# Optimization experiments

Measured on AMD Instinct MI355X. Metric: run time of the kernel, lower is better.

The kernel has to match this reference:

```python
import jax, jax.numpy as jnp
import numpy as np

N, D, Q, C_IN, C = 8192, 32, 4096, 128, 256
EPS = 1e-5

def _bn(h, g, b):
    # training-mode BatchNorm1d (biased variance, as torch uses for normalization)
    mu = h.mean(0)
    var = ((h - mu) ** 2).mean(0)
    return (h - mu) * jax.lax.rsqrt(var + EPS) * g + b

def setup_inputs():
    key = jax.random.key(0)
    cnt = iter(range(1000))
    def w(shape, s=0.05):
        return jax.random.normal(jax.random.fold_in(key, next(cnt)), shape, jnp.float32) * s
    ones = lambda n: jnp.ones((n,), jnp.float32)
    zeros = lambda n: jnp.zeros((n,), jnp.float32)
    rng = np.random.default_rng(0)
    block = N // D
    # padded neighbor table: rows sorted & duplicate-free (one neighbor per id-block)
    nbr_np = (np.arange(D)[None, :] * block + rng.integers(0, block, size=(N, D))).astype(np.int64)
    src = np.repeat(np.arange(N, dtype=np.int64), D)
    edge_index = jnp.asarray(np.stack([src, nbr_np.reshape(-1)]))
    E = edge_index.shape[1]
    C2 = 2 * C
    return {
        'x': w((N, C_IN), 1.0),
        'edge_index': edge_index,
        'edge_weight': jax.random.uniform(jax.random.fold_in(key, 999), (E,), jnp.float32, 0.5, 1.5),
        'edge_label_index': jnp.asarray(rng.integers(0, N, size=(2, Q)).astype(np.int64)),
        'nbr': jnp.asarray(nbr_np),
        'pe_gamma': ones(C_IN), 'pe_beta': zeros(C_IN),
        'W_pe': w((C_IN, C)), 'b_pe': zeros(C),
        'W_gcn': w((C, C)), 'b_gcn': zeros(C), 'bn1_g': ones(C), 'bn1_b': zeros(C),
        'Wq': w((C, C)), 'bq': zeros(C), 'Wk': w((C, C)), 'bk': zeros(C),
        'Wv': w((C, C)), 'bv': zeros(C), 'Wo': w((C, C)), 'bo': zeros(C),
        'bn2_g': ones(C), 'bn2_b': zeros(C),
        'W_m1': w((C, C2)), 'b_m1': zeros(C2), 'W_m2': w((C2, C)), 'b_m2': zeros(C),
        'bn3_g': ones(C), 'bn3_b': zeros(C),
        'W_cm': w((C, C)), 'b_cm': zeros(C), 'W_sm': w((C, C)), 'b_sm': zeros(C),
        'W_o1': w((C2, C)), 'b_o1': zeros(C), 'bno_g': ones(C), 'bno_b': zeros(C),
        'W_o2': w((C, 1)), 'b_o2': zeros(1),
        't': jnp.ones((), jnp.float32),
    }

def reference(x, edge_index, edge_weight, edge_label_index, nbr,
              pe_gamma, pe_beta, W_pe, b_pe,
              W_gcn, b_gcn, bn1_g, bn1_b,
              Wq, bq, Wk, bk, Wv, bv, Wo, bo, bn2_g, bn2_b,
              W_m1, b_m1, W_m2, b_m2, bn3_g, bn3_b,
              W_cm, b_cm, W_sm, b_sm,
              W_o1, b_o1, bno_g, bno_b, W_o2, b_o2, t):
    src, dst = edge_index[0], edge_index[1]
    h = _bn(x, pe_gamma, pe_beta) @ W_pe + b_pe                       # [N, C]
    # --- GPSConv layer: local GCN (self-loops) + global attention + MLP ---
    deg = jnp.zeros((N,), h.dtype).at[dst].add(edge_weight) + 1.0     # self-loop weight 1
    dinv = jax.lax.rsqrt(deg)
    hw = h @ W_gcn
    coef = dinv[src] * edge_weight * dinv[dst]
    agg = jnp.zeros_like(hw).at[dst].add(hw[src] * coef[:, None])
    local = agg + hw * (dinv * dinv)[:, None] + b_gcn
    h1 = _bn(local + h, bn1_g, bn1_b)
    q = h @ Wq + bq; k = h @ Wk + bk; v = h @ Wv + bv
    attn = jax.nn.softmax((q @ k.T) / jnp.sqrt(jnp.float32(C)), axis=-1)  # [N, N]
    h2 = _bn((attn @ v) @ Wo + bo + h, bn2_g, bn2_b)
    z = h1 + h2
    z = _bn(z + jax.nn.relu(z @ W_m1 + b_m1) @ W_m2 + b_m2, bn3_g, bn3_b)  # content features
    # --- structure: common-neighbor intersection + per-channel softmax aggregation ---
    s_nbr = nbr[edge_label_index[1]]        # [Q, D] sorted neighbors of source
    t_nbr = nbr[edge_label_index[0]]        # [Q, D] sorted neighbors of target
    pos = jnp.minimum(jax.vmap(jnp.searchsorted)(s_nbr, t_nbr), D - 1)
    mask = jnp.take_along_axis(s_nbr, pos, axis=1) == t_nbr           # common-neighbor mask
    zg = z[t_nbr]                           # [Q, D, C]
    m3 = mask[:, :, None]
    scores = jnp.where(m3, t * zg, -1e30)
    e = jnp.where(m3, jnp.exp(scores - jnp.max(scores, axis=1, keepdims=True)), 0.0)
    alpha = e / jnp.maximum(e.sum(axis=1, keepdims=True), 1e-12)
    structure = (alpha * zg).sum(axis=1)    # [Q, C]; zero rows when no common nbrs
    # --- predictor ---
    content = z[edge_label_index[0]] * z[edge_label_index[1]]
    hcat = jnp.concatenate([content @ W_cm + b_cm, structure @ W_sm + b_sm], axis=-1)
    hmid = jax.nn.relu(_bn(hcat @ W_o1 + b_o1, bno_g, bno_b))
    return hmid @ W_o2 + b_o2               # [Q, 1]
```

## Files before the change

kernel.cpp:

```cpp
#include <hip/hip_runtime.h>
#include <hip/hip_bf16.h>

using bf16 = __hip_bfloat16;
typedef __attribute__((ext_vector_type(8))) short short8;
typedef __attribute__((ext_vector_type(4))) float f32x4;
typedef __attribute__((ext_vector_type(4))) unsigned short us4;

#define NN 8192
#define DD 32
#define QQ 4096
#define CINN 128
#define CH 256
#define EE (NN*DD)
#define MBYTE ((size_t)1024*1024)
#define KB ((size_t)1024)

__device__ __forceinline__ short f2bf(float f){
  bf16 h = __float2bfloat16(f);
  return *reinterpret_cast<short*>(&h);
}
__device__ __forceinline__ float bf2f(unsigned short s){
  unsigned int u = ((unsigned int)s) << 16;
  return __uint_as_float(u);
}
__device__ __forceinline__ void gl_lds16(const void* g, void* l){
  __builtin_amdgcn_global_load_lds(
      (const __attribute__((address_space(1))) void*)g,
      (__attribute__((address_space(3))) void*)l, 16, 0, 0);
}

__global__ void k_prep(float* stats, int nstats, int* cnt,
                       const float* __restrict__ bq, const float* __restrict__ bk,
                       const float* __restrict__ bv, float* __restrict__ bcat){
  int i = blockIdx.x*256 + threadIdx.x;
  if (i < 1024){
    float v = 0.f;
    if (i >= 768)      v = bv[i-768];
    else if (i >= 512) v = bk[i-512];
    else if (i >= 256) v = bq[i-256]*0.0625f;
    bcat[i] = v;
  }
  int j = i - 1024;
  if (j >= 0 && j < nstats) stats[j] = 0.f;
  int k2 = j - nstats;
  if (k2 >= 0 && k2 < NN) cnt[k2] = 0;
}

struct WPack {
  const float* src[11];
  bf16* dst[11];
  int K[11];
  int N[11];
  float sc[11];
  int cum[12];
};
__global__ void k_wconv_all(WPack p){
  int idx = blockIdx.x*256 + threadIdx.x;
  if (idx >= p.cum[11]) return;
  int w = 0;
#pragma unroll
  for (int i = 1; i < 11; i++) w += (idx >= p.cum[i]) ? 1 : 0;
  int loc = idx - p.cum[w];
  int K = p.K[w], N = p.N[w];
  int n = loc / K, k = loc - n*K;
  p.dst[w][loc] = __float2bfloat16(p.src[w][(size_t)k*N + n] * p.sc[w]);
}

__global__ void k_bnstats(const float* __restrict__ X, float* __restrict__ sums, int M, int C){
  int c = threadIdx.x;
  float s = 0.f, s2 = 0.f;
  for (int r = blockIdx.x; r < M; r += gridDim.x){
    float v = X[(size_t)r*C + c];
    s += v; s2 += v*v;
  }
  atomicAdd(&sums[c], s);
  atomicAdd(&sums[C+c], s2);
}

__global__ void k_bnapply(const float* __restrict__ X, const float* __restrict__ sums,
                          const float* __restrict__ g, const float* __restrict__ b,
                          const float* __restrict__ addin, const bf16* __restrict__ addinb,
                          float* __restrict__ outf, bf16* __restrict__ outb,
                          int M, int Cm1, int relu){
  int idx = blockIdx.x*256 + threadIdx.x;
  int c = idx & Cm1;
  int C = Cm1 + 1;
  float mu = sums[c] / (float)M;
  float var = sums[C+c] / (float)M - mu*mu;
  float rs = rsqrtf(var + 1e-5f);
  float v = (X[idx] - mu)*rs*g[c] + b[c];
  if (addin) v += addin[idx];
  if (addinb) v += __bfloat162float(addinb[idx]);
  if (relu) v = fmaxf(v, 0.f);
  if (outf) outf[idx] = v;
  if (outb) outb[idx] = __float2bfloat16(v);
}

template<int KCH>
__global__ __launch_bounds__(256)
void k_gemm(const bf16* __restrict__ A, const bf16* __restrict__ BT,
            const float* __restrict__ bias,
            const float* __restrict__ resid, const bf16* __restrict__ residb,
            float* __restrict__ Cf, bf16* __restrict__ Cb,
            int Ncols, int ldc, int relu,
            const bf16* __restrict__ A2, const bf16* __restrict__ BT2,
            const float* __restrict__ bias2, int half, int colbase2,
            float* __restrict__ stats)
{
  constexpr int K = KCH*32;
  int bid = blockIdx.x;
  const bf16* Ause = A;
  const bf16* BTu = BT;
  const float* bi = bias;
  int colbase = 0;
  if (A2 && bid >= half){ Ause = A2; BTu = BT2; bi = bias2; bid -= half; colbase = colbase2; }
  const int row0 = bid*16;
  const int wid = threadIdx.x >> 6;
  const int lane = threadIdx.x & 63;
  const int lr = lane & 15, lg = lane >> 4;
  short8 af[KCH];
  const short* Arow = (const short*)Ause + (size_t)(row0+lr)*K + lg*8;
#pragma unroll
  for (int c2 = 0; c2 < KCH; c2++) af[c2] = *(const short8*)(Arow + c2*32);
  const int ntiles = Ncols >> 4;
  for (int ct = wid; ct < ntiles; ct += 4){
    f32x4 acc = {0.f,0.f,0.f,0.f};
    const short* Brow = (const short*)BTu + (size_t)(ct*16+lr)*K + lg*8;
#pragma unroll
    for (int c2 = 0; c2 < KCH; c2++){
      short8 bfr = *(const short8*)(Brow + c2*32);
      acc = __builtin_amdgcn_mfma_f32_16x16x32_bf16(af[c2], bfr, acc, 0, 0, 0);
    }
    int col = colbase + ct*16 + lr;
    float bvv = bi ? bi[ct*16+lr] : 0.f;
    float vv[4];
#pragma unroll
    for (int r = 0; r < 4; r++){
      int row = row0 + lg*4 + r;
      size_t o = (size_t)row*ldc + col;
      float v = acc[r] + bvv;
      if (resid) v += resid[o];
      if (residb) v += __bfloat162float(residb[o]);
      if (relu) v = fmaxf(v, 0.f);
      if (Cf) Cf[o] = v;
      if (Cb) Cb[o] = __float2bfloat16(v);
      vv[r] = v;
    }
    if (stats){
      float s  = vv[0]+vv[1]+vv[2]+vv[3];
      float s2 = vv[0]*vv[0]+vv[1]*vv[1]+vv[2]*vv[2]+vv[3]*vv[3];
      s  += __shfl_xor(s, 16, 64);  s  += __shfl_xor(s, 32, 64);
      s2 += __shfl_xor(s2, 16, 64); s2 += __shfl_xor(s2, 32, 64);
      if (lg == 0){
        atomicAdd(&stats[col], s);
        atomicAdd(&stats[CH + col], s2);
      }
    }
  }
}

template<int KCH>
__global__ __launch_bounds__(256)
void k_gemm2(const bf16* __restrict__ A, const bf16* __restrict__ BT,
             const float* __restrict__ bias,
             const float* __restrict__ resid, const bf16* __restrict__ residb,
             float* __restrict__ Cf, bf16* __restrict__ Cb,
             int ncolsh, int ldc, int relu,
             int halfblocks, int colshift,
             float* __restrict__ stats)
{
  constexpr int K = KCH*32;
  int bid = blockIdx.x;
  int colbase = 0;
  if (bid >= halfblocks){ bid -= halfblocks; colbase = colshift; }
  const int row0 = bid*32;
  const int wid = threadIdx.x >> 6;
  const int lane = threadIdx.x & 63;
  const int lr = lane & 15, lg = lane >> 4;
  short8 af0[KCH], af1[KCH];
  const short* Arow0 = (const short*)A + (size_t)(row0+lr)*K + lg*8;
  const short* Arow1 = Arow0 + 16*K;
#pragma unroll
  for (int c2 = 0; c2 < KCH; c2++){
    af0[c2] = *(const short8*)(Arow0 + c2*32);
    af1[c2] = *(const short8*)(Arow1 + c2*32);
  }
  const int ntiles = ncolsh >> 4;
  for (int ct = wid; ct < ntiles; ct += 4){
    f32x4 a0 = {0.f,0.f,0.f,0.f}, a1 = {0.f,0.f,0.f,0.f};
    const short* Brow = (const short*)BT + (size_t)(colbase + ct*16 + lr)*K + lg*8;
#pragma unroll
    for (int c2 = 0; c2 < KCH; c2++){
      short8 bfr = *(const short8*)(Brow + c2*32);
      a0 = __builtin_amdgcn_mfma_f32_16x16x32_bf16(af0[c2], bfr, a0, 0, 0, 0);
      a1 = __builtin_amdgcn_mfma_f32_16x16x32_bf16(af1[c2], bfr, a1, 0, 0, 0);
    }
    int col = colbase + ct*16 + lr;
    float bvv = bias ? bias[col] : 0.f;
    float vv0[4], vv1[4];
#pragma unroll
    for (int r = 0; r < 4; r++){
      int row = row0 + lg*4 + r;
      size_t o0 = (size_t)row*ldc + col;
      size_t o1 = (size_t)(row+16)*ldc + col;
      float v0 = a0[r] + bvv;
      float v1 = a1[r] + bvv;
      if (resid){ v0 += resid[o0]; v1 += resid[o1]; }
      if (residb){ v0 += __bfloat162float(residb[o0]); v1 += __bfloat162float(residb[o1]); }
      if (relu){ v0 = fmaxf(v0, 0.f); v1 = fmaxf(v1, 0.f); }
      if (Cf){ Cf[o0] = v0; Cf[o1] = v1; }
      if (Cb){ Cb[o0] = __float2bfloat16(v0); Cb[o1] = __float2bfloat16(v1); }
      vv0[r] = v0; vv1[r] = v1;
    }
    if (stats){
      float s  = vv0[0]+vv0[1]+vv0[2]+vv0[3] + vv1[0]+vv1[1]+vv1[2]+vv1[3];
      float s2 = vv0[0]*vv0[0]+vv0[1]*vv0[1]+vv0[2]*vv0[2]+vv0[3]*vv0[3]
               + vv1[0]*vv1[0]+vv1[1]*vv1[1]+vv1[2]*vv1[2]+vv1[3]*vv1[3];
      s  += __shfl_xor(s, 16, 64);  s  += __shfl_xor(s, 32, 64);
      s2 += __shfl_xor(s2, 16, 64); s2 += __shfl_xor(s2, 32, 64);
      if (lg == 0){
        atomicAdd(&stats[col], s);
        atomicAdd(&stats[CH + col], s2);
      }
    }
  }
}

__global__ void k_hist(const int* __restrict__ dst, int* __restrict__ cnt){
  int e = blockIdx.x*256 + threadIdx.x;
  if (e < EE) atomicAdd(&cnt[dst[e]], 1);
}

__global__ void k_scan(const int* __restrict__ cnt, int* __restrict__ off, int* __restrict__ woff){
  __shared__ int s[256];
  int t = threadIdx.x;
  int base = t*32;
  int local[32];
  int sum = 0;
#pragma unroll
  for (int i = 0; i < 32; i++){ local[i] = sum; sum += cnt[base+i]; }
  s[t] = sum;
  __syncthreads();
  if (t == 0){
    int run = 0;
    for (int i = 0; i < 256; i++){ int v = s[i]; s[i] = run; run += v; }
  }
  __syncthreads();
  int b = s[t];
#pragma unroll
  for (int i = 0; i < 32; i++){ off[base+i] = b + local[i]; woff[base+i] = b + local[i]; }
  if (t == 255) off[8192] = EE;
}

__global__ void k_fill(const int* __restrict__ dst, int* __restrict__ woff, int* __restrict__ elist){
  int e = blockIdx.x*256 + threadIdx.x;
  if (e < EE){
    int p = atomicAdd(&woff[dst[e]], 1);
    elist[p] = e;
  }
}

__global__ __launch_bounds__(256)
void k_degcsr(const int* __restrict__ off, const int* __restrict__ elist,
              const float* __restrict__ ew, float* __restrict__ dinv){
  int n = blockIdx.x*4 + (threadIdx.x >> 6);
  int lane = threadIdx.x & 63;
  int o0 = off[n], o1 = off[n+1];
  float s = 0.f;
  for (int j = o0 + lane; j < o1; j += 64) s += ew[elist[j]];
#pragma unroll
  for (int o = 32; o; o >>= 1) s += __shfl_xor(s, o, 64);
  if (lane == 0) dinv[n] = rsqrtf(s + 1.0f);
}

__global__ __launch_bounds__(256)
void k_gather(const int* __restrict__ off, const int* __restrict__ elist,
              const float* __restrict__ ew, const float* __restrict__ dinv,
              const unsigned short* __restrict__ hwq, const unsigned short* __restrict__ hb16,
              const float* __restrict__ bgcn, float* __restrict__ y1){
  int n = blockIdx.x*4 + (threadIdx.x >> 6);
  int lane = threadIdx.x & 63;
  int o0 = off[n], o1 = off[n+1];
  float dn = dinv[n];
  f32x4 acc = {0.f,0.f,0.f,0.f};
  for (int j = o0; j < o1; j++){
    int e = elist[j];
    int s = e >> 5;
    float coef = dinv[s]*ew[e]*dn;
    us4 v = *(const us4*)(hwq + (size_t)s*1024 + lane*4);
    acc[0] += bf2f(v[0])*coef; acc[1] += bf2f(v[1])*coef;
    acc[2] += bf2f(v[2])*coef; acc[3] += bf2f(v[3])*coef;
  }
  us4 hv = *(const us4*)(hwq + (size_t)n*1024 + lane*4);
  us4 hn = *(const us4*)(hb16 + (size_t)n*CH + lane*4);
  f32x4 bg  = ((const f32x4*)bgcn)[lane];
  float dd = dn*dn;
  f32x4 o;
  o[0] = acc[0] + bf2f(hv[0])*dd + bg[0] + bf2f(hn[0]);
  o[1] = acc[1] + bf2f(hv[1])*dd + bg[1] + bf2f(hn[1]);
  o[2] = acc[2] + bf2f(hv[2])*dd + bg[2] + bf2f(hn[2]);
  o[3] = acc[3] + bf2f(hv[3])*dd + bg[3] + bf2f(hn[3]);
  ((f32x4*)(y1 + (size_t)n*CH))[lane] = o;
}

__global__ __launch_bounds__(256)
void k_transpose(const bf16* __restrict__ in, bf16* __restrict__ out, int istride){
  __shared__ short tile[32][33];
  int bx = blockIdx.x & 7;
  int by = blockIdx.x >> 3;
  int tx = threadIdx.x & 31, ty = threadIdx.x >> 5;
  const short* inp = (const short*)in;
  short* outp = (short*)out;
#pragma unroll
  for (int i = 0; i < 4; i++)
    tile[ty + i*8][tx] = inp[(size_t)(by*32 + ty + i*8)*istride + bx*32 + tx];
  __syncthreads();
#pragma unroll
  for (int i = 0; i < 4; i++)
    outp[(size_t)(bx*32 + ty + i*8)*8192 + by*32 + tx] = tile[tx][ty + i*8];
}

__global__ __launch_bounds__(256, 2)
void k_attn9(const bf16* __restrict__ QKV, const bf16* __restrict__ VT,
             bf16* __restrict__ Opart, float* __restrict__ Lpart)
{
  __shared__ char lds[75776];
  const int wid = threadIdx.x >> 6, lane = threadIdx.x & 63;
  const int lr = lane & 15, lg = lane >> 4;
  const int qt = blockIdx.x >> 3, sp = blockIdx.x & 7;
  const int q0 = qt*128 + wid*32;
  const int kbase = sp*1024;
  const float M0 = 8.f;

  short8 qf[2][8];
#pragma unroll
  for (int qs = 0; qs < 2; qs++){
    const short* Qrow = (const short*)QKV + 256 + (size_t)(q0 + qs*16 + lr)*1024 + lg*8;
#pragma unroll
    for (int c = 0; c < 8; c++) qf[qs][c] = *(const short8*)(Qrow + c*32);
  }

  const char* kS[4];
  const char* vS[4];
  int ldst[4];
#pragma unroll
  for (int i = 0; i < 4; i++){
    int L = wid*1024 + i*4096 + lane*16;
    int r = L >> 9, b = L & 511;
    kS[i] = (const char*)QKV + (size_t)(kbase + r)*2048 + 1024 + (b ^ ((r&7)<<4));
    int j = L >> 7, b2 = L & 127;
    int bp2 = b2 ^ ((j&7)<<4);
    int dim = 2*j + (bp2 >= 64 ? 1 : 0);
    vS[i] = (const char*)VT + ((size_t)dim*8192 + kbase)*2 + (bp2 & 63);
    ldst[i] = wid*1024 + i*4096;
  }

  f32x4 acc[2][16];
#pragma unroll
  for (int qs = 0; qs < 2; qs++)
#pragma unroll
    for (int dt = 0; dt < 16; dt++) acc[qs][dt] = {0.f,0.f,0.f,0.f};
  float ls[2][4];
#pragma unroll
  for (int qs = 0; qs < 2; qs++)
#pragma unroll
    for (int r = 0; r < 4; r++) ls[qs][r] = 0.f;

  char* sPw = lds + 65536 + wid*2560;

#pragma unroll
  for (int i = 0; i < 4; i++){
    gl_lds16(kS[i], lds + ldst[i]);           kS[i] += 65536;
    gl_lds16(vS[i], lds + 16384 + ldst[i]);   vS[i] += 64;
  }
  __syncthreads();

  for (int t = 0; t < 32; t++){
    const int buf = t & 1;
    if (t < 31){
      char* nb = lds + (buf^1)*32768;
#pragma unroll
      for (int i = 0; i < 4; i++){
        gl_lds16(kS[i], nb + ldst[i]);           kS[i] += 65536;
        gl_lds16(vS[i], nb + 16384 + ldst[i]);   vS[i] += 64;
      }
    }
    const char* bK = lds + buf*32768;
    const char* bV = bK + 16384;

    {
      f32x4 s0 = {0.f,0.f,0.f,0.f}, s1 = {0.f,0.f,0.f,0.f};
      __builtin_amdgcn_s_setprio(1);
#pragma unroll
      for (int c = 0; c < 8; c++){
        int g = c*64 + lg*16;
        short8 kf0 = *(const short8*)(bK + lr*512 + (g ^ ((lr&7)<<4)));
        s0 = __builtin_amdgcn_mfma_f32_16x16x32_bf16(qf[0][c], kf0, s0, 0, 0, 0);
        short8 kf1 = *(const short8*)(bK + (16+lr)*512 + (g ^ ((lr&7)<<4)));
        s1 = __builtin_amdgcn_mfma_f32_16x16x32_bf16(qf[0][c], kf1, s1, 0, 0, 0);
      }
      __builtin_amdgcn_s_setprio(0);
#pragma unroll
      for (int r = 0; r < 4; r++){
        float p0 = __expf(s0[r] - M0);
        float p1 = __expf(s1[r] - M0);
        ls[0][r] += p0 + p1;
        int prow = lg*4 + r;
        *(short*)(sPw + prow*80 + lr*2)      = f2bf(p0);
        *(short*)(sPw + prow*80 + 32 + lr*2) = f2bf(p1);
      }
    }
    {
      f32x4 s0 = {0.f,0.f,0.f,0.f}, s1 = {0.f,0.f,0.f,0.f};
      __builtin_amdgcn_s_setprio(1);
#pragma unroll
      for (int c = 0; c < 8; c++){
        int g = c*64 + lg*16;
        short8 kf0 = *(const short8*)(bK + lr*512 + (g ^ ((lr&7)<<4)));
        s0 = __builtin_amdgcn_mfma_f32_16x16x32_bf16(qf[1][c], kf0, s0, 0, 0, 0);
        short8 kf1 = *(const short8*)(bK + (16+lr)*512 + (g ^ ((lr&7)<<4)));
        s1 = __builtin_amdgcn_mfma_f32_16x16x32_bf16(qf[1][c], kf1, s1, 0, 0, 0);
      }
      __builtin_amdgcn_s_setprio(0);
#pragma unroll
      for (int r = 0; r < 4; r++){
        float p0 = __expf(s0[r] - M0);
        float p1 = __expf(s1[r] - M0);
        ls[1][r] += p0 + p1;
        int prow = lg*4 + r;
        *(short*)(sPw + 1280 + prow*80 + lr*2)      = f2bf(p0);
        *(short*)(sPw + 1280 + prow*80 + 32 + lr*2) = f2bf(p1);
      }
    }
    __builtin_amdgcn_sched_barrier(0);
    short8 pf0 = *(const short8*)(sPw + lr*80 + lg*16);
    short8 pf1 = *(const short8*)(sPw + 1280 + lr*80 + lg*16);
    __builtin_amdgcn_s_setprio(1);
#pragma unroll
    for (int dt = 0; dt < 16; dt++){
      int d = dt*16 + lr;
      int j = d >> 1;
      int gp = (d&1)*64 + lg*16;
      short8 vf = *(const short8*)(bV + j*128 + (gp ^ ((j&7)<<4)));
      acc[0][dt] = __builtin_amdgcn_mfma_f32_16x16x32_bf16(pf0, vf, acc[0][dt], 0, 0, 0);
      acc[1][dt] = __builtin_amdgcn_mfma_f32_16x16x32_bf16(pf1, vf, acc[1][dt], 0, 0, 0);
    }
    __builtin_amdgcn_s_setprio(0);
    __syncthreads();
  }

#pragma unroll
  for (int qs = 0; qs < 2; qs++){
#pragma unroll
    for (int r = 0; r < 4; r++){
#pragma unroll
      for (int off = 1; off < 16; off <<= 1) ls[qs][r] += __shfl_xor(ls[qs][r], off, 64);
    }
  }
  if (lr == 0){
#pragma unroll
    for (int qs = 0; qs < 2; qs++){
#pragma unroll
      for (int r = 0; r < 4; r++){
        int row = q0 + qs*16 + lg*4 + r;
        Lpart[sp*NN + row] = ls[qs][r];
      }
    }
  }
  char* reg = lds + wid*8192;
  size_t ob = (size_t)sp*NN*CH;
#pragma unroll
  for (int qs = 0; qs < 2; qs++){
#pragma unroll
    for (int dt = 0; dt < 16; dt++){
#pragma unroll
      for (int r = 0; r < 4; r++){
        int qr = lg*4 + r;
        *(short*)(reg + qr*512 + ((dt*32 + lr*2) ^ ((qr&7)<<4))) = f2bf(acc[qs][dt][r]);
      }
    }
    __syncthreads();
#pragma unroll
    for (int rnd = 0; rnd < 8; rnd++){
      int qr = rnd*2 + (lane >> 5);
      int colb = (lane & 31)*16;
      short8 v = *(const short8*)(reg + qr*512 + (colb ^ ((qr&7)<<4)));
      *(short8*)((short*)Opart + ob + (size_t)(q0 + qs*16 + qr)*CH + colb/2) = v;
    }
    __syncthreads();
  }
}

__global__ __launch_bounds__(256)
void k_merge8(const bf16* __restrict__ Opart, const float* __restrict__ Lp,
              bf16* __restrict__ out){
  int tid = blockIdx.x*256 + threadIdx.x;
  int q = tid >> 5;
  int cb = (tid & 31) * 8;
  float den = 0.f;
#pragma unroll
  for (int s = 0; s < 8; s++) den += Lp[s*NN + q];
  float inv = 1.f / den;
  float o[8];
#pragma unroll
  for (int j = 0; j < 8; j++) o[j] = 0.f;
#pragma unroll
  for (int s = 0; s < 8; s++){
    short8 v = *(const short8*)((const short*)Opart + (size_t)s*NN*CH + (size_t)q*CH + cb);
#pragma unroll
    for (int j = 0; j < 8; j++) o[j] += bf2f((unsigned short)v[j]);
  }
  short8 res;
#pragma unroll
  for (int j = 0; j < 8; j++) res[j] = f2bf(o[j]*inv);
  *(short8*)((short*)out + (size_t)q*CH + cb) = res;
}

__global__ __launch_bounds__(256)
void k_head(const int* __restrict__ eli, const int* __restrict__ nbr,
            const float* __restrict__ y3, const float* __restrict__ stat3,
            const float* __restrict__ g3, const float* __restrict__ b3,
            const float* __restrict__ tptr,
            bf16* __restrict__ outc, bf16* __restrict__ outs){
  __shared__ int tn[32];
  __shared__ int msk[32];
  int q = blockIdx.x;
  int a0 = eli[q], b0 = eli[QQ + q];
  if (threadIdx.x < 32){
    int d = threadIdx.x;
    int a = nbr[(size_t)a0*DD + d];
    int s = nbr[(size_t)b0*DD + d];
    tn[d] = a;
    msk[d] = (a == s);
  }
  __syncthreads();
  int c = threadIdx.x;
  float mu = stat3[c] / (float)NN;
  float var = stat3[CH + c] / (float)NN - mu*mu;
  float rs = rsqrtf(var + 1e-5f);
  float sc = rs*g3[c];
  float sh = b3[c] - mu*sc;
  float za = y3[(size_t)a0*CH + c]*sc + sh;
  float zb = y3[(size_t)b0*CH + c]*sc + sh;
  outc[(size_t)q*CH + c] = __float2bfloat16(za*zb);
  float tval = tptr[0];
  float vmax = -1e30f;
  float zg[32];
#pragma unroll
  for (int d = 0; d < 32; d++){
    float v = msk[d] ? (y3[(size_t)tn[d]*CH + c]*sc + sh) : 0.f;
    zg[d] = v;
    float scv = msk[d] ? tval*v : -1e30f;
    vmax = fmaxf(vmax, scv);
  }
  float esum = 0.f, wsum = 0.f;
#pragma unroll
  for (int d = 0; d < 32; d++){
    float e = msk[d] ? __expf(tval*zg[d] - vmax) : 0.f;
    esum += e;
    wsum += e*zg[d];
  }
  outs[(size_t)q*CH + c] = __float2bfloat16(wsum / fmaxf(esum, 1e-12f));
}

__global__ __launch_bounds__(256)
void k_final(const bf16* __restrict__ hmid, const float* __restrict__ w,
             const float* __restrict__ b, float* __restrict__ out){
  int r = blockIdx.x*4 + (threadIdx.x >> 6);
  int lane = threadIdx.x & 63;
  float s = 0.f;
#pragma unroll
  for (int i = 0; i < 4; i++){
    int c = lane + 64*i;
    s += __bfloat162float(hmid[(size_t)r*CH + c]) * w[c];
  }
#pragma unroll
  for (int off = 32; off; off >>= 1) s += __shfl_xor(s, off, 64);
  if (lane == 0) out[r] = s + b[0];
}

extern "C" void kernel_launch(void* const* d_in, const int* in_sizes, int n_in,
                              void* d_out, int out_size, void* d_ws, size_t ws_size,
                              hipStream_t stream)
{
  const float* x      = (const float*)d_in[0];
  const int*   eidx   = (const int*)d_in[1];
  const float* ew     = (const float*)d_in[2];
  const int*   eli    = (const int*)d_in[3];
  const int*   nbr    = (const int*)d_in[4];
  const float* pe_g   = (const float*)d_in[5];
  const float* pe_b   = (const float*)d_in[6];
  const float* W_pe   = (const float*)d_in[7];
  const float* b_pe   = (const float*)d_in[8];
  const float* W_gcn  = (const float*)d_in[9];
  const float* b_gcn  = (const float*)d_in[10];
  const float* bn1_g  = (const float*)d_in[11];
  const float* bn1_b  = (const float*)d_in[12];
  const float* Wq     = (const float*)d_in[13];
  const float* bq     = (const float*)d_in[14];
  const float* Wk     = (const float*)d_in[15];
  const float* bk     = (const float*)d_in[16];
  const float* Wv     = (const float*)d_in[17];
  const float* bvv    = (const float*)d_in[18];
  const float* Wo     = (const float*)d_in[19];
  const float* bo     = (const float*)d_in[20];
  const float* bn2_g  = (const float*)d_in[21];
  const float* bn2_b  = (const float*)d_in[22];
  const float* W_m1   = (const float*)d_in[23];
  const float* b_m1   = (const float*)d_in[24];
  const float* W_m2   = (const float*)d_in[25];
  const float* b_m2   = (const float*)d_in[26];
  const float* bn3_g  = (const float*)d_in[27];
  const float* bn3_b  = (const float*)d_in[28];
  const float* W_cm   = (const float*)d_in[29];
  const float* b_cm   = (const float*)d_in[30];
  const float* W_sm   = (const float*)d_in[31];
  const float* b_sm   = (const float*)d_in[32];
  const float* W_o1   = (const float*)d_in[33];
  const float* b_o1   = (const float*)d_in[34];
  const float* bno_g  = (const float*)d_in[35];
  const float* bno_b  = (const float*)d_in[36];
  const float* W_o2   = (const float*)d_in[37];
  const float* b_o2   = (const float*)d_in[38];
  const float* tptr   = (const float*)d_in[39];

  if (ws_size < 64*MBYTE) return;
  char* ws = (char*)d_ws;

  bf16* WgcnT = (bf16*)(ws + 0);
  bf16* WqT   = (bf16*)(ws + 128*KB);
  bf16* WkT   = (bf16*)(ws + 256*KB);
  bf16* WvT   = (bf16*)(ws + 384*KB);
  bf16* WpeT  = (bf16*)(ws + 512*KB);
  bf16* Wm1T  = (bf16*)(ws + 576*KB);
  bf16* Wm2T  = (bf16*)(ws + 832*KB);
  bf16* WcmT  = (bf16*)(ws + 1088*KB);
  bf16* WsmT  = (bf16*)(ws + 1216*KB);
  bf16* Wo1T  = (bf16*)(ws + 1344*KB);
  bf16* WoT   = (bf16*)(ws + 1600*KB);

  float* stat_x = (float*)(ws + 2*MBYTE);
  float* stat1  = (float*)(ws + 2*MBYTE + 1*KB);
  float* stat2  = (float*)(ws + 2*MBYTE + 3*KB);
  float* stat3  = (float*)(ws + 2*MBYTE + 5*KB);
  float* stato  = (float*)(ws + 2*MBYTE + 7*KB);
  float* deg    = (float*)(ws + 2*MBYTE + 16*KB);
  float* bcat   = (float*)(ws + 2*MBYTE + 64*KB);
  int*   cnt    = (int*)(ws + 2*MBYTE + 128*KB);
  int*   off    = (int*)(ws + 2*MBYTE + 160*KB);
  int*   woff   = (int*)(ws + 2*MBYTE + 224*KB);
  int*   elist  = (int*)(ws + 2*MBYTE + 288*KB);
  float* Lpart  = (float*)(ws + 2*MBYTE + 1664*KB);

  bf16*  hb    = (bf16*)(ws + 4*MBYTE);
  bf16*  xn    = (bf16*)(ws + 8*MBYTE);
  float* aggb  = (float*)(ws + 10*MBYTE);
  bf16*  OpartB= (bf16*)(ws + 8*MBYTE);
  bf16*  vT    = (bf16*)(ws + 40*MBYTE);
  bf16*  qkvg  = (bf16*)(ws + 44*MBYTE);
  bf16*  h1b   = (bf16*)(ws + 60*MBYTE);
  bf16*  attnb = (bf16*)(ws + 40*MBYTE);
  float* y2    = (float*)(ws + 8*MBYTE);
  float* zf    = (float*)(ws + 16*MBYTE);
  bf16*  zb    = (bf16*)(ws + 24*MBYTE);
  bf16*  midb  = (bf16*)(ws + 28*MBYTE);
  float* y3    = (float*)(ws + 44*MBYTE);
  bf16*  contb = (bf16*)(ws + 8*MBYTE);
  bf16*  strub = (bf16*)(ws + 10*MBYTE);
  bf16*  hcat  = (bf16*)(ws + 12*MBYTE);
  float* y4    = (float*)(ws + 16*MBYTE);
  bf16*  hmid  = (bf16*)(ws + 20*MBYTE);

  const int* dstp = eidx + EE;

  k_prep<<<(1024 + 12288 + NN + 255)/256, 256, 0, stream>>>((float*)(ws + 2*MBYTE), 12288, cnt, bq, bk, bvv, bcat);

  {
    WPack p;
    const float* s[11] = {W_gcn, Wq, Wk, Wv, W_pe, W_m1, W_m2, W_cm, W_sm, W_o1, Wo};
    bf16* dsts[11] = {WgcnT, WqT, WkT, WvT, WpeT, Wm1T, Wm2T, WcmT, WsmT, Wo1T, WoT};
    int Ks[11] = {256,256,256,256,128,256,512,256,256,512,256};
    int Ns[11] = {256,256,256,256,256,512,256,256,256,256,256};
    float scs[11] = {1.f,0.0625f,1.f,1.f,1.f,1.f,1.f,1.f,1.f,1.f,1.f};
    int c = 0;
    for (int i = 0; i < 11; i++){
      p.src[i]=s[i]; p.dst[i]=dsts[i]; p.K[i]=Ks[i]; p.N[i]=Ns[i]; p.sc[i]=scs[i];
      p.cum[i]=c; c += Ks[i]*Ns[i];
    }
    p.cum[11]=c;
    k_wconv_all<<<(c+255)/256, 256, 0, stream>>>(p);
  }

  k_hist<<<EE/256, 256, 0, stream>>>(dstp, cnt);
  k_scan<<<1, 256, 0, stream>>>(cnt, off, woff);
  k_fill<<<EE/256, 256, 0, stream>>>(dstp, woff, elist);
  k_degcsr<<<NN/4, 256, 0, stream>>>(off, elist, ew, deg);

  k_bnstats<<<256, 128, 0, stream>>>(x, stat_x, NN, CINN);
  k_bnapply<<<NN*CINN/256, 256, 0, stream>>>(x, stat_x, pe_g, pe_b, nullptr, nullptr, nullptr, xn, NN, CINN-1, 0);

  k_gemm2<4><<<512, 256, 0, stream>>>(xn, WpeT, b_pe, nullptr, nullptr, nullptr, hb, 128, 256, 0,
                                       256, 128, nullptr);

  k_gemm2<8><<<512, 256, 0, stream>>>(hb, WgcnT, bcat, nullptr, nullptr, nullptr, qkvg, 512, 1024, 0,
                                       256, 512, nullptr);

  k_gather<<<NN/4, 256, 0, stream>>>(off, elist, ew, deg,
                                      (const unsigned short*)qkvg, (const unsigned short*)hb, b_gcn, aggb);

  k_bnstats<<<256, 256, 0, stream>>>(aggb, stat1, NN, CH);
  k_bnapply<<<NN*CH/256, 256, 0, stream>>>(aggb, stat1, bn1_g, bn1_b, nullptr, nullptr, nullptr, h1b, NN, CH-1, 0);

  k_transpose<<<2048, 256, 0, stream>>>(qkvg + 768, vT, 1024);

  k_attn9<<<512, 256, 0, stream>>>(qkvg, vT, OpartB, Lpart);
  k_merge8<<<NN*32/256, 256, 0, stream>>>(OpartB, Lpart, attnb);

  k_gemm2<8><<<512, 256, 0, stream>>>(attnb, WoT, bo, nullptr, hb, y2, nullptr, 128, 256, 0,
                                       256, 128, stat2);

  k_bnapply<<<NN*CH/256, 256, 0, stream>>>(y2, stat2, bn2_g, bn2_b, nullptr, h1b, zf, zb, NN, CH-1, 0);

  k_gemm2<8><<<512, 256, 0, stream>>>(zb, Wm1T, b_m1, nullptr, nullptr, nullptr, midb, 256, 512, 1,
                                       256, 256, nullptr);
  k_gemm2<16><<<512, 256, 0, stream>>>(midb, Wm2T, b_m2, zf, nullptr, y3, nullptr, 128, 256, 0,
                                        256, 128, stat3);

  k_head<<<QQ, 256, 0, stream>>>(eli, nbr, y3, stat3, bn3_g, bn3_b, tptr, contb, strub);

  k_gemm<8><<<2*(QQ/16), 256, 0, stream>>>(contb, WcmT, b_cm, nullptr, nullptr, nullptr, hcat, 256, 512, 0,
                                            strub, WsmT, b_sm, QQ/16, 256, nullptr);

  k_gemm2<16><<<256, 256, 0, stream>>>(hcat, Wo1T, b_o1, nullptr, nullptr, y4, nullptr, 128, 256, 0,
                                        128, 128, stato);
  k_bnapply<<<QQ*CH/256, 256, 0, stream>>>(y4, stato, bno_g, bno_b, nullptr, nullptr, nullptr, hmid, QQ, CH-1, 1);

  k_final<<<QQ/4, 256, 0, stream>>>(hmid, W_o2, b_o2, (float*)d_out);
}
```

Measured before the change: 376.2 us.

## Fuse prep kernels, defer BN1 into z kernel, fold final BN into head

Merges the prep and weight-conversion launches into one kernel. The GCN gather now writes bf16 instead of fp32, and its BN stats are read from bf16. BN1 is no longer applied in its own pass: it is applied together with BN2 and the residual inside a new k_bnz kernel. The last BN+ReLU is folded into k_final, and the MLP residual now reads bf16 z instead of fp32 z. This removes several launches and full-tensor round trips, at the cost of extra bf16 rounding on the aggregated features and the residual.

```diff
diff --git a/kernel.cpp b/kernel.cpp
--- a/kernel.cpp
+++ b/kernel.cpp
@@ -29,23 +29,6 @@
       (__attribute__((address_space(3))) void*)l, 16, 0, 0);
 }
 
-__global__ void k_prep(float* stats, int nstats, int* cnt,
-                       const float* __restrict__ bq, const float* __restrict__ bk,
-                       const float* __restrict__ bv, float* __restrict__ bcat){
-  int i = blockIdx.x*256 + threadIdx.x;
-  if (i < 1024){
-    float v = 0.f;
-    if (i >= 768)      v = bv[i-768];
-    else if (i >= 512) v = bk[i-512];
-    else if (i >= 256) v = bq[i-256]*0.0625f;
-    bcat[i] = v;
-  }
-  int j = i - 1024;
-  if (j >= 0 && j < nstats) stats[j] = 0.f;
-  int k2 = j - nstats;
-  if (k2 >= 0 && k2 < NN) cnt[k2] = 0;
-}
-
 struct WPack {
   const float* src[11];
   bf16* dst[11];
@@ -54,12 +37,27 @@
   float sc[11];
   int cum[12];
 };
-__global__ void k_wconv_all(WPack p){
-  int idx = blockIdx.x*256 + threadIdx.x;
+__global__ void k_prepw(WPack p, float* stats, int nstats, int* cnt,
+                        const float* __restrict__ bq, const float* __restrict__ bk,
+                        const float* __restrict__ bv, float* __restrict__ bcat){
+  int i = blockIdx.x*256 + threadIdx.x;
+  if (i < 1024){
+    float v = 0.f;
+    if (i >= 768)      v = bv[i-768];
+    else if (i >= 512) v = bk[i-512];
+    else if (i >= 256) v = bq[i-256]*0.0625f;
+    bcat[i] = v;
+    return;
+  }
+  int j = i - 1024;
+  if (j < nstats){ stats[j] = 0.f; return; }
+  int k2 = j - nstats;
+  if (k2 < NN){ cnt[k2] = 0; return; }
+  int idx = k2 - NN;
   if (idx >= p.cum[11]) return;
   int w = 0;
 #pragma unroll
-  for (int i = 1; i < 11; i++) w += (idx >= p.cum[i]) ? 1 : 0;
+  for (int t = 1; t < 11; t++) w += (idx >= p.cum[t]) ? 1 : 0;
   int loc = idx - p.cum[w];
   int K = p.K[w], N = p.N[w];
   int n = loc / K, k = loc - n*K;
@@ -77,11 +75,20 @@
   atomicAdd(&sums[C+c], s2);
 }
 
+__global__ void k_bnstats_b(const bf16* __restrict__ X, float* __restrict__ sums, int M, int C){
+  int c = threadIdx.x;
+  float s = 0.f, s2 = 0.f;
+  for (int r = blockIdx.x; r < M; r += gridDim.x){
+    float v = __bfloat162float(X[(size_t)r*C + c]);
+    s += v; s2 += v*v;
+  }
+  atomicAdd(&sums[c], s);
+  atomicAdd(&sums[C+c], s2);
+}
+
 __global__ void k_bnapply(const float* __restrict__ X, const float* __restrict__ sums,
                           const float* __restrict__ g, const float* __restrict__ b,
-                          const float* __restrict__ addin, const bf16* __restrict__ addinb,
-                          float* __restrict__ outf, bf16* __restrict__ outb,
-                          int M, int Cm1, int relu){
+                          bf16* __restrict__ outb, int M, int Cm1){
   int idx = blockIdx.x*256 + threadIdx.x;
   int c = idx & Cm1;
   int C = Cm1 + 1;
@@ -89,23 +96,34 @@
   float var = sums[C+c] / (float)M - mu*mu;
   float rs = rsqrtf(var + 1e-5f);
   float v = (X[idx] - mu)*rs*g[c] + b[c];
-  if (addin) v += addin[idx];
-  if (addinb) v += __bfloat162float(addinb[idx]);
-  if (relu) v = fmaxf(v, 0.f);
-  if (outf) outf[idx] = v;
-  if (outb) outb[idx] = __float2bfloat16(v);
+  outb[idx] = __float2bfloat16(v);
+}
+
+__global__ void k_bnz(const float* __restrict__ y2, const float* __restrict__ stat2,
+                      const float* __restrict__ g2, const float* __restrict__ b2,
+                      const bf16* __restrict__ y1b, const float* __restrict__ stat1,
+                      const float* __restrict__ g1, const float* __restrict__ b1,
+                      bf16* __restrict__ zb){
+  int idx = blockIdx.x*256 + threadIdx.x;
+  int c = idx & 255;
+  float mu2 = stat2[c] / (float)NN;
+  float var2 = stat2[CH+c] / (float)NN - mu2*mu2;
+  float rs2 = rsqrtf(var2 + 1e-5f);
+  float v2 = (y2[idx] - mu2)*rs2*g2[c] + b2[c];
+  float mu1 = stat1[c] / (float)NN;
+  float var1 = stat1[CH+c] / (float)NN - mu1*mu1;
+  float rs1 = rsqrtf(var1 + 1e-5f);
+  float v1 = (__bfloat162float(y1b[idx]) - mu1)*rs1*g1[c] + b1[c];
+  zb[idx] = __float2bfloat16(v1 + v2);
 }
 
 template<int KCH>
 __global__ __launch_bounds__(256)
 void k_gemm(const bf16* __restrict__ A, const bf16* __restrict__ BT,
             const float* __restrict__ bias,
-            const float* __restrict__ resid, const bf16* __restrict__ residb,
-            float* __restrict__ Cf, bf16* __restrict__ Cb,
-            int Ncols, int ldc, int relu,
+            bf16* __restrict__ Cb, int ldc,
             const bf16* __restrict__ A2, const bf16* __restrict__ BT2,
-            const float* __restrict__ bias2, int half, int colbase2,
-            float* __restrict__ stats)
+            const float* __restrict__ bias2, int half, int colbase2)
 {
   constexpr int K = KCH*32;
   int bid = blockIdx.x;
@@ -122,7 +140,7 @@
   const short* Arow = (const short*)Ause + (size_t)(row0+lr)*K + lg*8;
 #pragma unroll
   for (int c2 = 0; c2 < KCH; c2++) af[c2] = *(const short8*)(Arow + c2*32);
-  const int ntiles = Ncols >> 4;
+  const int ntiles = 256 >> 4;
   for (int ct = wid; ct < ntiles; ct += 4){
     f32x4 acc = {0.f,0.f,0.f,0.f};
     const short* Brow = (const short*)BTu + (size_t)(ct*16+lr)*K + lg*8;
@@ -133,28 +151,12 @@
     }
     int col = colbase + ct*16 + lr;
     float bvv = bi ? bi[ct*16+lr] : 0.f;
-    float vv[4];
 #pragma unroll
     for (int r = 0; r < 4; r++){
       int row = row0 + lg*4 + r;
       size_t o = (size_t)row*ldc + col;
       float v = acc[r] + bvv;
-      if (resid) v += resid[o];
-      if (residb) v += __bfloat162float(residb[o]);
-      if (relu) v = fmaxf(v, 0.f);
-      if (Cf) Cf[o] = v;
-      if (Cb) Cb[o] = __float2bfloat16(v);
-      vv[r] = v;
-    }
-    if (stats){
-      float s  = vv[0]+vv[1]+vv[2]+vv[3];
-      float s2 = vv[0]*vv[0]+vv[1]*vv[1]+vv[2]*vv[2]+vv[3]*vv[3];
-      s  += __shfl_xor(s, 16, 64);  s  += __shfl_xor(s, 32, 64);
-      s2 += __shfl_xor(s2, 16, 64); s2 += __shfl_xor(s2, 32, 64);
-      if (lg == 0){
-        atomicAdd(&stats[col], s);
-        atomicAdd(&stats[CH + col], s2);
-      }
+      Cb[o] = __float2bfloat16(v);
     }
   }
 }
@@ -277,7 +279,7 @@
 void k_gather(const int* __restrict__ off, const int* __restrict__ elist,
               const float* __restrict__ ew, const float* __restrict__ dinv,
               const unsigned short* __restrict__ hwq, const unsigned short* __restrict__ hb16,
-              const float* __restrict__ bgcn, float* __restrict__ y1){
+              const float* __restrict__ bgcn, bf16* __restrict__ y1b){
   int n = blockIdx.x*4 + (threadIdx.x >> 6);
   int lane = threadIdx.x & 63;
   int o0 = off[n], o1 = off[n+1];
@@ -295,12 +297,12 @@
   us4 hn = *(const us4*)(hb16 + (size_t)n*CH + lane*4);
   f32x4 bg  = ((const f32x4*)bgcn)[lane];
   float dd = dn*dn;
-  f32x4 o;
-  o[0] = acc[0] + bf2f(hv[0])*dd + bg[0] + bf2f(hn[0]);
-  o[1] = acc[1] + bf2f(hv[1])*dd + bg[1] + bf2f(hn[1]);
-  o[2] = acc[2] + bf2f(hv[2])*dd + bg[2] + bf2f(hn[2]);
-  o[3] = acc[3] + bf2f(hv[3])*dd + bg[3] + bf2f(hn[3]);
-  ((f32x4*)(y1 + (size_t)n*CH))[lane] = o;
+  us4 o;
+  o[0] = (unsigned short)f2bf(acc[0] + bf2f(hv[0])*dd + bg[0] + bf2f(hn[0]));
+  o[1] = (unsigned short)f2bf(acc[1] + bf2f(hv[1])*dd + bg[1] + bf2f(hn[1]));
+  o[2] = (unsigned short)f2bf(acc[2] + bf2f(hv[2])*dd + bg[2] + bf2f(hn[2]));
+  o[3] = (unsigned short)f2bf(acc[3] + bf2f(hv[3])*dd + bg[3] + bf2f(hn[3]));
+  *(us4*)((unsigned short*)y1b + (size_t)n*CH + lane*4) = o;
 }
 
 __global__ __launch_bounds__(256)
@@ -564,19 +566,26 @@
 }
 
 __global__ __launch_bounds__(256)
-void k_final(const bf16* __restrict__ hmid, const float* __restrict__ w,
-             const float* __restrict__ b, float* __restrict__ out){
+void k_final(const float* __restrict__ y4, const float* __restrict__ stato,
+             const float* __restrict__ g, const float* __restrict__ b,
+             const float* __restrict__ w, const float* __restrict__ bo2,
+             float* __restrict__ out){
   int r = blockIdx.x*4 + (threadIdx.x >> 6);
   int lane = threadIdx.x & 63;
   float s = 0.f;
 #pragma unroll
   for (int i = 0; i < 4; i++){
     int c = lane + 64*i;
-    s += __bfloat162float(hmid[(size_t)r*CH + c]) * w[c];
+    float mu = stato[c] / (float)QQ;
+    float var = stato[CH+c] / (float)QQ - mu*mu;
+    float rs = rsqrtf(var + 1e-5f);
+    float v = (y4[(size_t)r*CH + c] - mu)*rs*g[c] + b[c];
+    v = fmaxf(v, 0.f);
+    s += v * w[c];
   }
 #pragma unroll
   for (int off = 32; off; off >>= 1) s += __shfl_xor(s, off, 64);
-  if (lane == 0) out[r] = s + b[0];
+  if (lane == 0) out[r] = s + bo2[0];
 }
 
 extern "C" void kernel_launch(void* const* d_in, const int* in_sizes, int n_in,
@@ -654,14 +663,12 @@
 
   bf16*  hb    = (bf16*)(ws + 4*MBYTE);
   bf16*  xn    = (bf16*)(ws + 8*MBYTE);
-  float* aggb  = (float*)(ws + 10*MBYTE);
   bf16*  OpartB= (bf16*)(ws + 8*MBYTE);
   bf16*  vT    = (bf16*)(ws + 40*MBYTE);
   bf16*  qkvg  = (bf16*)(ws + 44*MBYTE);
-  bf16*  h1b   = (bf16*)(ws + 60*MBYTE);
+  bf16*  y1b   = (bf16*)(ws + 60*MBYTE);
   bf16*  attnb = (bf16*)(ws + 40*MBYTE);
   float* y2    = (float*)(ws + 8*MBYTE);
-  float* zf    = (float*)(ws + 16*MBYTE);
   bf16*  zb    = (bf16*)(ws + 24*MBYTE);
   bf16*  midb  = (bf16*)(ws + 28*MBYTE);
   float* y3    = (float*)(ws + 44*MBYTE);
@@ -669,11 +676,8 @@
   bf16*  strub = (bf16*)(ws + 10*MBYTE);
   bf16*  hcat  = (bf16*)(ws + 12*MBYTE);
   float* y4    = (float*)(ws + 16*MBYTE);
-  bf16*  hmid  = (bf16*)(ws + 20*MBYTE);
 
   const int* dstp = eidx + EE;
-
-  k_prep<<<(1024 + 12288 + NN + 255)/256, 256, 0, stream>>>((float*)(ws + 2*MBYTE), 12288, cnt, bq, bk, bvv, bcat);
 
   {
     WPack p;
@@ -688,7 +692,8 @@
       p.cum[i]=c; c += Ks[i]*Ns[i];
     }
     p.cum[11]=c;
-    k_wconv_all<<<(c+255)/256, 256, 0, stream>>>(p);
+    int total = 1024 + 12288 + NN + c;
+    k_prepw<<<(total+255)/256, 256, 0, stream>>>(p, (float*)(ws + 2*MBYTE), 12288, cnt, bq, bk, bvv, bcat);
   }
 
   k_hist<<<EE/256, 256, 0, stream>>>(dstp, cnt);
@@ -697,7 +702,7 @@
   k_degcsr<<<NN/4, 256, 0, stream>>>(off, elist, ew, deg);
 
   k_bnstats<<<256, 128, 0, stream>>>(x, stat_x, NN, CINN);
-  k_bnapply<<<NN*CINN/256, 256, 0, stream>>>(x, stat_x, pe_g, pe_b, nullptr, nullptr, nullptr, xn, NN, CINN-1, 0);
+  k_bnapply<<<NN*CINN/256, 256, 0, stream>>>(x, stat_x, pe_g, pe_b, xn, NN, CINN-1);
 
   k_gemm2<4><<<512, 256, 0, stream>>>(xn, WpeT, b_pe, nullptr, nullptr, nullptr, hb, 128, 256, 0,
                                        256, 128, nullptr);
@@ -706,10 +711,9 @@
                                        256, 512, nullptr);
 
   k_gather<<<NN/4, 256, 0, stream>>>(off, elist, ew, deg,
-                                      (const unsigned short*)qkvg, (const unsigned short*)hb, b_gcn, aggb);
-
-  k_bnstats<<<256, 256, 0, stream>>>(aggb, stat1, NN, CH);
-  k_bnapply<<<NN*CH/256, 256, 0, stream>>>(aggb, stat1, bn1_g, bn1_b, nullptr, nullptr, nullptr, h1b, NN, CH-1, 0);
+                                      (const unsigned short*)qkvg, (const unsigned short*)hb, b_gcn, y1b);
+
+  k_bnstats_b<<<256, 256, 0, stream>>>(y1b, stat1, NN, CH);
 
   k_transpose<<<2048, 256, 0, stream>>>(qkvg + 768, vT, 1024);
 
@@ -719,21 +723,20 @@
   k_gemm2<8><<<512, 256, 0, stream>>>(attnb, WoT, bo, nullptr, hb, y2, nullptr, 128, 256, 0,
                                        256, 128, stat2);
 
-  k_bnapply<<<NN*CH/256, 256, 0, stream>>>(y2, stat2, bn2_g, bn2_b, nullptr, h1b, zf, zb, NN, CH-1, 0);
+  k_bnz<<<NN*CH/256, 256, 0, stream>>>(y2, stat2, bn2_g, bn2_b, y1b, stat1, bn1_g, bn1_b, zb);
 
   k_gemm2<8><<<512, 256, 0, stream>>>(zb, Wm1T, b_m1, nullptr, nullptr, nullptr, midb, 256, 512, 1,
                                        256, 256, nullptr);
-  k_gemm2<16><<<512, 256, 0, stream>>>(midb, Wm2T, b_m2, zf, nullptr, y3, nullptr, 128, 256, 0,
+  k_gemm2<16><<<512, 256, 0, stream>>>(midb, Wm2T, b_m2, nullptr, zb, y3, nullptr, 128, 256, 0,
                                         256, 128, stat3);
 
   k_head<<<QQ, 256, 0, stream>>>(eli, nbr, y3, stat3, bn3_g, bn3_b, tptr, contb, strub);
 
-  k_gemm<8><<<2*(QQ/16), 256, 0, stream>>>(contb, WcmT, b_cm, nullptr, nullptr, nullptr, hcat, 256, 512, 0,
-                                            strub, WsmT, b_sm, QQ/16, 256, nullptr);
+  k_gemm<8><<<2*(QQ/16), 256, 0, stream>>>(contb, WcmT, b_cm, hcat, 512,
+                                            strub, WsmT, b_sm, QQ/16, 256);
 
   k_gemm2<16><<<256, 256, 0, stream>>>(hcat, Wo1T, b_o1, nullptr, nullptr, y4, nullptr, 128, 256, 0,
                                         128, 128, stato);
-  k_bnapply<<<QQ*CH/256, 256, 0, stream>>>(y4, stato, bno_g, bno_b, nullptr, nullptr, nullptr, hmid, QQ, CH-1, 1);
-
-  k_final<<<QQ/4, 256, 0, stream>>>(hmid, W_o2, b_o2, (float*)d_out);
-}
+
+  k_final<<<QQ/4, 256, 0, stream>>>(y4, stato, bno_g, bno_b, W_o2, b_o2, (float*)d_out);
+}
```

Measured after the change: 360.1 us. -4.3%, faster.
